# Kernel optimization log

Hardware: AMD Instinct MI355X
Metric: run time of the kernel (lower is better)

## Reference

```python
import jax, jax.numpy as jnp
import numpy as np

D_MODEL = 1024
NUM_HEADS = 16
DEPTH = D_MODEL // NUM_HEADS


def setup_inputs() -> dict:
    key = jax.random.key(0)
    ks = jax.random.split(key, 10)
    B, LQ, LK = 4, 2048, 2048
    # xavier_uniform bound for square [d,d] weight
    bound = float(np.sqrt(6.0 / (D_MODEL + D_MODEL)))
    def w(k):
        return jax.random.uniform(k, (D_MODEL, D_MODEL), jnp.float32, -bound, bound)
    return {
        "query": jax.random.normal(ks[0], (B, LQ, D_MODEL), jnp.float32),
        "value": jax.random.normal(ks[1], (B, LK, D_MODEL), jnp.float32),
        "wq": w(ks[2]), "bq": jnp.zeros((D_MODEL,), jnp.float32),
        "wk": w(ks[3]), "bk": jnp.zeros((D_MODEL,), jnp.float32),
        "wv": w(ks[4]), "bv": jnp.zeros((D_MODEL,), jnp.float32),
        "wo": w(ks[5]), "bo": jnp.zeros((D_MODEL,), jnp.float32),
    }


def _split_heads(x, B):
    # [B, L, d_model] -> [B, H, L, depth]
    return x.reshape(B, -1, NUM_HEADS, DEPTH).transpose(0, 2, 1, 3)


def reference(query, value, wq, bq, wk, bk, wv, bv, wo, bo):
    B = query.shape[0]
    # torch nn.Linear: y = x @ W.T + b
    q = _split_heads(query @ wq.T + bq, B)          # [B,H,Lq,depth]
    k = _split_heads(value @ wk.T + bk, B)          # [B,H,Lk,depth]
    v = _split_heads(value @ wv.T + bv, B)          # [B,H,Lk,depth]
    scale = jnp.sqrt(jnp.asarray(DEPTH, dtype=q.dtype))
    scores = jnp.einsum("bhqd,bhkd->bhqk", q, k) / scale
    attn = jax.nn.softmax(scores, axis=-1)
    ctx = jnp.einsum("bhqk,bhkd->bhqd", attn, v)    # [B,H,Lq,depth]
    ctx = ctx.transpose(0, 2, 1, 3).reshape(B, -1, D_MODEL)
    return ctx @ wo.T + bo
```

## Files before the change

kernel.cpp:

```cpp
#include <hip/hip_runtime.h>
#include <hip/hip_bf16.h>

typedef unsigned short u16;
typedef unsigned int u32;
typedef __attribute__((ext_vector_type(8))) short bf16x8;
typedef __attribute__((ext_vector_type(4))) float f32x4;

#define MFMA16(a, b, c) __builtin_amdgcn_mfma_f32_16x16x32_bf16(a, b, c, 0, 0, 0)

#define QSCALE 0.18033688011112042f

__device__ inline u16 f2b(float f) {
    union { float f; unsigned int i; } v;
    v.f = f;
    unsigned int r = v.i + 0x7fffu + ((v.i >> 16) & 1u);
    return (u16)(r >> 16);
}
__device__ inline u32 fbits(float f) {
    union { float f; u32 i; } v; v.f = f; return v.i;
}
__device__ inline u32 pack2_trunc(float f0, float f1) {
    return __builtin_amdgcn_perm(fbits(f1), fbits(f0), 0x07060302u);
}

__device__ inline void glds16(const u16* g, u16* l) {
    __builtin_amdgcn_global_load_lds(
        (const __attribute__((address_space(1))) unsigned int*)g,
        (__attribute__((address_space(3))) unsigned int*)l, 16, 0, 0);
}

__global__ __launch_bounds__(256) void cvt_all(
    const float* __restrict__ q, const float* __restrict__ v,
    const float* __restrict__ wq, const float* __restrict__ wk,
    const float* __restrict__ wv, const float* __restrict__ wo,
    u16* __restrict__ qb, u16* __restrict__ vb,
    u16* __restrict__ wqb, u16* __restrict__ wkb,
    u16* __restrict__ wvb, u16* __restrict__ wob)
{
    int flat = blockIdx.x;
    const float* x; u16* y; int off;
    if (flat < 8192) {
        x = flat < 4096 ? q : v;
        y = flat < 4096 ? qb : vb;
        off = flat & 4095;
    } else {
        int s = (flat - 8192) >> 9;
        off = (flat - 8192) & 511;
        x = s == 0 ? wq : (s == 1 ? wk : (s == 2 ? wv : wo));
        y = s == 0 ? wqb : (s == 1 ? wkb : (s == 2 ? wvb : wob));
    }
    int i = (off * 256 + threadIdx.x) * 8;
    float4 a = *(const float4*)(x + i);
    float4 b = *(const float4*)(x + i + 4);
    u16 o[8] = { f2b(a.x), f2b(a.y), f2b(a.z), f2b(a.w),
                 f2b(b.x), f2b(b.y), f2b(b.z), f2b(b.w) };
    *(uint4*)(y + i) = *(uint4*)o;
}

__global__ __launch_bounds__(256) void gemm_proj(
    const u16* __restrict__ qb, const u16* __restrict__ vb,
    const u16* __restrict__ wqb, const u16* __restrict__ wkb,
    const u16* __restrict__ wvb,
    const float* __restrict__ bq, const float* __restrict__ bk,
    const float* __restrict__ bv,
    u16* __restrict__ Qp, u16* __restrict__ Kp, u16* __restrict__ Vp,
    int M, int K)
{
    const int flat = blockIdx.x;
    const int xcd = flat & 7, idx = flat >> 3;
    const int mt  = xcd * 8 + (idx & 7);
    const int yy  = idx >> 3;
    const int sel = yy >> 3;
    const int n0 = (yy & 7) * 128;
    const u16* A = sel ? vb : qb;
    const u16* W = sel == 0 ? wqb : (sel == 1 ? wkb : wvb);
    const float* bias = sel == 0 ? bq : (sel == 1 ? bk : bv);
    u16* C = sel == 0 ? Qp : (sel == 1 ? Kp : Vp);
    const float cscale = sel == 0 ? QSCALE : 1.0f;

    __shared__ __align__(16) u16 As[128 * 32];
    __shared__ __align__(16) u16 Bs[128 * 32];

    const int tid  = threadIdx.x;
    const int wave = tid >> 6, lane = tid & 63;
    const int quad = lane >> 4, l16 = lane & 15;
    const int m0 = mt * 128;
    const int wm = (wave >> 1) * 64, wn = (wave & 1) * 64;
    const int r0 = lane >> 2;
    const int c0 = (lane & 3) * 8;

    f32x4 acc[4][4] = {};

    for (int k0 = 0; k0 < K; k0 += 32) {
        __syncthreads();
        {
            int ra = wave * 16 + r0;
            glds16(&A[(size_t)(m0 + ra) * K + k0 + c0],      &As[ra * 32 + c0]);
            glds16(&A[(size_t)(m0 + 64 + ra) * K + k0 + c0], &As[(64 + ra) * 32 + c0]);
            glds16(&W[(size_t)(n0 + ra) * K + k0 + c0],      &Bs[ra * 32 + c0]);
            glds16(&W[(size_t)(n0 + 64 + ra) * K + k0 + c0], &Bs[(64 + ra) * 32 + c0]);
        }
        __syncthreads();

        bf16x8 af[4], bfr[4];
#pragma unroll
        for (int mi = 0; mi < 4; ++mi)
            af[mi] = *(const bf16x8*)(&As[(wm + mi * 16 + l16) * 32 + quad * 8]);
#pragma unroll
        for (int ni = 0; ni < 4; ++ni)
            bfr[ni] = *(const bf16x8*)(&Bs[(wn + ni * 16 + l16) * 32 + quad * 8]);
#pragma unroll
        for (int mi = 0; mi < 4; ++mi)
#pragma unroll
            for (int ni = 0; ni < 4; ++ni)
                acc[mi][ni] = MFMA16(af[mi], bfr[ni], acc[mi][ni]);
    }

#pragma unroll
    for (int mi = 0; mi < 4; ++mi) {
#pragma unroll
        for (int ni = 0; ni < 4; ++ni) {
            int col = n0 + wn + ni * 16 + l16;
            float bv2 = bias[col];
#pragma unroll
            for (int r = 0; r < 4; ++r) {
                int row = m0 + wm + mi * 16 + quad * 4 + r;
                C[(size_t)row * 1024 + col] = f2b((acc[mi][ni][r] + bv2) * cscale);
            }
        }
    }
}

__global__ __launch_bounds__(256) void gemm_out(
    const u16* __restrict__ A, const u16* __restrict__ B,
    const float* __restrict__ bias, float* __restrict__ C,
    int M, int N, int K)
{
    __shared__ __align__(16) u16 As[128 * 32];
    __shared__ __align__(16) u16 Bs[128 * 32];

    const int flat = blockIdx.x;
    const int xcd = flat & 7, idx = flat >> 3;
    const int mt  = xcd * 8 + (idx & 7);
    const int m0 = mt * 128, n0 = (idx >> 3) * 128;

    const int tid  = threadIdx.x;
    const int wave = tid >> 6, lane = tid & 63;
    const int quad = lane >> 4, l16 = lane & 15;
    const int wm = (wave >> 1) * 64, wn = (wave & 1) * 64;
    const int r0 = lane >> 2;
    const int c0 = (lane & 3) * 8;

    f32x4 acc[4][4] = {};

    for (int k0 = 0; k0 < K; k0 += 32) {
        __syncthreads();
        {
            int ra = wave * 16 + r0;
            glds16(&A[(size_t)(m0 + ra) * K + k0 + c0],      &As[ra * 32 + c0]);
            glds16(&A[(size_t)(m0 + 64 + ra) * K + k0 + c0], &As[(64 + ra) * 32 + c0]);
            glds16(&B[(size_t)(n0 + ra) * K + k0 + c0],      &Bs[ra * 32 + c0]);
            glds16(&B[(size_t)(n0 + 64 + ra) * K + k0 + c0], &Bs[(64 + ra) * 32 + c0]);
        }
        __syncthreads();

        bf16x8 af[4], bfr[4];
#pragma unroll
        for (int mi = 0; mi < 4; ++mi)
            af[mi] = *(const bf16x8*)(&As[(wm + mi * 16 + l16) * 32 + quad * 8]);
#pragma unroll
        for (int ni = 0; ni < 4; ++ni)
            bfr[ni] = *(const bf16x8*)(&Bs[(wn + ni * 16 + l16) * 32 + quad * 8]);
#pragma unroll
        for (int mi = 0; mi < 4; ++mi)
#pragma unroll
            for (int ni = 0; ni < 4; ++ni)
                acc[mi][ni] = MFMA16(af[mi], bfr[ni], acc[mi][ni]);
    }

#pragma unroll
    for (int mi = 0; mi < 4; ++mi) {
#pragma unroll
        for (int ni = 0; ni < 4; ++ni) {
            int col = n0 + wn + ni * 16 + l16;
            float bv = bias[col];
#pragma unroll
            for (int r = 0; r < 4; ++r) {
                int row = m0 + wm + mi * 16 + quad * 4 + r;
                C[(size_t)row * N + col] = acc[mi][ni][r] + bv;
            }
        }
    }
}

__global__ __launch_bounds__(256) void transpose_v(
    const u16* __restrict__ Vp, u16* __restrict__ VT)
{
    __shared__ u16 T[64 * 66];
    const int tid = threadIdx.x;
    const int l0 = blockIdx.x * 64, d0 = blockIdx.y * 64, b = blockIdx.z;

#pragma unroll
    for (int i = 0; i < 2; ++i) {
        int ch = tid + i * 256;
        int lrow = ch >> 3, c8 = (ch & 7) * 8;
        uint4 vv = *(const uint4*)(&Vp[((size_t)b * 2048 + l0 + lrow) * 1024 + d0 + c8]);
        const u16* vp = (const u16*)&vv;
#pragma unroll
        for (int j = 0; j < 8; ++j) T[lrow * 66 + c8 + j] = vp[j];
    }
    __syncthreads();
#pragma unroll
    for (int i = 0; i < 2; ++i) {
        int ch = tid + i * 256;
        int drow = ch >> 3, l8 = (ch & 7) * 8;
        u16 o[8];
#pragma unroll
        for (int j = 0; j < 8; ++j) o[j] = T[(l8 + j) * 66 + drow];
        *(uint4*)(&VT[((size_t)b * 1024 + d0 + drow) * 2048 + l0 + l8]) = *(uint4*)o;
    }
}

__global__ __launch_bounds__(256, 4) void attn(
    const u16* __restrict__ Q, const u16* __restrict__ K,
    const u16* __restrict__ VT, u16* __restrict__ O,
    int LQ, int LK)
{
    const int tid  = threadIdx.x;
    const int wave = tid >> 6, lane = tid & 63;
    const int quad = lane >> 4, l16 = lane & 15;
    const int flat = blockIdx.x;
    const int xcd = flat & 7, slot = flat >> 3;
    const int bh = xcd * 8 + (slot >> 4);
    const int q0 = (slot & 15) * 128;
    const int b = bh >> 4, h = bh & 15;
    const size_t qbase = ((size_t)b * LQ + q0) * 1024 + h * 64;
    const size_t kbase = ((size_t)b * LK) * 1024 + h * 64;
    const size_t vtbase = ((size_t)b * 1024 + h * 64) * 2048;

    __shared__ __align__(16) u16 Ks[64 * 72];
    __shared__ __align__(16) u16 VTs[64 * 72];
    __shared__ __align__(16) u16 Ps[4][32 * 40];

    bf16x8 qf[2][2];
#pragma unroll
    for (int mi = 0; mi < 2; ++mi)
#pragma unroll
        for (int ks = 0; ks < 2; ++ks)
            qf[mi][ks] = *(const bf16x8*)(
                &Q[qbase + (size_t)(wave * 32 + mi * 16 + l16) * 1024 + ks * 32 + quad * 8]);

    const bf16x8 vones = { 0x3F80, 0x3F80, 0x3F80, 0x3F80,
                           0x3F80, 0x3F80, 0x3F80, 0x3F80 };

    f32x4 oacc[2][5] = {};

    for (int kt = 0; kt < LK; kt += 64) {
        __syncthreads();
#pragma unroll
        for (int i = 0; i < 2; ++i) {
            int ch = tid + i * 256;
            int row = ch >> 3, c8 = (ch & 7) * 8;
            *(uint4*)(&Ks[row * 72 + c8]) =
                *(const uint4*)(&K[kbase + (size_t)(kt + row) * 1024 + c8]);
            *(uint4*)(&VTs[row * 72 + c8]) =
                *(const uint4*)(&VT[vtbase + (size_t)row * 2048 + kt + c8]);
        }
        __syncthreads();

        f32x4 st[4][2] = {};
#pragma unroll
        for (int ks = 0; ks < 2; ++ks) {
            bf16x8 kf[4];
#pragma unroll
            for (int ni = 0; ni < 4; ++ni)
                kf[ni] = *(const bf16x8*)(&Ks[(ni * 16 + l16) * 72 + ks * 32 + quad * 8]);
            __builtin_amdgcn_s_setprio(1);
#pragma unroll
            for (int ni = 0; ni < 4; ++ni)
#pragma unroll
                for (int mi = 0; mi < 2; ++mi)
                    st[ni][mi] = MFMA16(kf[ni], qf[mi][ks], st[ni][mi]);
            __builtin_amdgcn_s_setprio(0);
        }

#pragma unroll
        for (int ks = 0; ks < 2; ++ks) {
#pragma unroll
            for (int mi = 0; mi < 2; ++mi)
#pragma unroll
                for (int ni2 = 0; ni2 < 2; ++ni2) {
                    const f32x4 s4 = st[ks * 2 + ni2][mi];
                    float p0 = __builtin_amdgcn_exp2f(s4[0]);
                    float p1 = __builtin_amdgcn_exp2f(s4[1]);
                    float p2 = __builtin_amdgcn_exp2f(s4[2]);
                    float p3 = __builtin_amdgcn_exp2f(s4[3]);
                    uint2 w;
                    w.x = pack2_trunc(p0, p1);
                    w.y = pack2_trunc(p2, p3);
                    *(uint2*)(&Ps[wave][(mi * 16 + l16) * 40 + ni2 * 16 + quad * 4]) = w;
                }

            bf16x8 vf[4];
#pragma unroll
            for (int nd = 0; nd < 4; ++nd)
                vf[nd] = *(const bf16x8*)(&VTs[(nd * 16 + l16) * 72 + ks * 32 + quad * 8]);
            __builtin_amdgcn_s_setprio(1);
#pragma unroll
            for (int mi = 0; mi < 2; ++mi) {
                bf16x8 pf = *(const bf16x8*)(&Ps[wave][(mi * 16 + l16) * 40 + quad * 8]);
#pragma unroll
                for (int nd = 0; nd < 4; ++nd)
                    oacc[mi][nd] = MFMA16(pf, vf[nd], oacc[mi][nd]);
                oacc[mi][4] = MFMA16(pf, vones, oacc[mi][4]);
            }
            __builtin_amdgcn_s_setprio(0);
        }
    }

#pragma unroll
    for (int mi = 0; mi < 2; ++mi)
#pragma unroll
        for (int r = 0; r < 4; ++r) {
            float inv = 1.0f / oacc[mi][4][r];
            int row = q0 + wave * 32 + mi * 16 + quad * 4 + r;
            size_t rb = ((size_t)b * LQ + row) * 1024 + h * 64;
#pragma unroll
            for (int nd = 0; nd < 4; ++nd)
                O[rb + nd * 16 + l16] = f2b(oacc[mi][nd][r] * inv);
        }
}

extern "C" void kernel_launch(void* const* d_in, const int* in_sizes, int n_in,
                              void* d_out, int out_size, void* d_ws, size_t ws_size,
                              hipStream_t stream) {
    const float* query = (const float*)d_in[0];
    const float* value = (const float*)d_in[1];
    const float* wq = (const float*)d_in[2];
    const float* bq = (const float*)d_in[3];
    const float* wk = (const float*)d_in[4];
    const float* bk = (const float*)d_in[5];
    const float* wv = (const float*)d_in[6];
    const float* bv = (const float*)d_in[7];
    const float* wo = (const float*)d_in[8];
    const float* bo = (const float*)d_in[9];

    const int B = 4, LQ = 2048, LK = 2048, D = 1024;
    const int M = B * LQ;
    const int mat = M * D;
    const int wsz = D * D;

    u16* ws  = (u16*)d_ws;
    u16* qb  = ws;
    u16* vb  = qb + mat;
    u16* wqb = vb + mat;
    u16* wkb = wqb + wsz;
    u16* wvb = wkb + wsz;
    u16* wob = wvb + wsz;
    u16* Qp  = wob + wsz;
    u16* Kp  = Qp + mat;
    u16* Vp  = Kp + mat;
    u16* VT  = Vp + mat;
    u16* Cp  = Vp;

    dim3 blk(256);

    cvt_all<<<dim3(10240), blk, 0, stream>>>(
        query, value, wq, wk, wv, wo, qb, vb, wqb, wkb, wvb, wob);

    gemm_proj<<<dim3(1536), blk, 0, stream>>>(
        qb, vb, wqb, wkb, wvb, bq, bk, bv, Qp, Kp, Vp, M, D);

    transpose_v<<<dim3(32, 16, 4), blk, 0, stream>>>(Vp, VT);

    attn<<<dim3(1024), blk, 0, stream>>>(Qp, Kp, VT, Cp, LQ, LK);

    gemm_out<<<dim3(512), blk, 0, stream>>>(Cp, wob, bo, (float*)d_out, M, D, D);
}
```

Baseline: 328.5 us.

## Fuse V transpose into projection epilogue and compute softmax row sums in VALU

The V projection GEMM now writes its output already transposed (VT layout) with 4-element packed stores, so the separate transpose_v kernel and its extra read/write pass over V disappear. Separately, the attention kernel drops the extra MFMA against a ones vector that produced the softmax denominator. It instead accumulates per-lane row sums of the truncated bf16 probabilities in registers and reduces them with cross-lane shuffles at the end. The risks are strided 8-byte stores in the GEMM epilogue and extra VALU work in the attention inner loop.

```diff
diff --git a/kernel.cpp b/kernel.cpp
--- a/kernel.cpp
+++ b/kernel.cpp
@@ -18,6 +18,9 @@
 }
 __device__ inline u32 fbits(float f) {
     union { float f; u32 i; } v; v.f = f; return v.i;
+}
+__device__ inline float bfloat(u32 b) {
+    union { u32 i; float f; } v; v.i = b; return v.f;
 }
 __device__ inline u32 pack2_trunc(float f0, float f1) {
     return __builtin_amdgcn_perm(fbits(f1), fbits(f0), 0x07060302u);
@@ -63,7 +66,7 @@
     const u16* __restrict__ wvb,
     const float* __restrict__ bq, const float* __restrict__ bk,
     const float* __restrict__ bv,
-    u16* __restrict__ Qp, u16* __restrict__ Kp, u16* __restrict__ Vp,
+    u16* __restrict__ Qp, u16* __restrict__ Kp, u16* __restrict__ VT,
     int M, int K)
 {
     const int flat = blockIdx.x;
@@ -75,7 +78,6 @@
     const u16* A = sel ? vb : qb;
     const u16* W = sel == 0 ? wqb : (sel == 1 ? wkb : wvb);
     const float* bias = sel == 0 ? bq : (sel == 1 ? bk : bv);
-    u16* C = sel == 0 ? Qp : (sel == 1 ? Kp : Vp);
     const float cscale = sel == 0 ? QSCALE : 1.0f;
 
     __shared__ __align__(16) u16 As[128 * 32];
@@ -116,16 +118,34 @@
                 acc[mi][ni] = MFMA16(af[mi], bfr[ni], acc[mi][ni]);
     }
 
-#pragma unroll
-    for (int mi = 0; mi < 4; ++mi) {
-#pragma unroll
-        for (int ni = 0; ni < 4; ++ni) {
-            int col = n0 + wn + ni * 16 + l16;
-            float bv2 = bias[col];
-#pragma unroll
-            for (int r = 0; r < 4; ++r) {
-                int row = m0 + wm + mi * 16 + quad * 4 + r;
-                C[(size_t)row * 1024 + col] = f2b((acc[mi][ni][r] + bv2) * cscale);
+    if (sel == 2) {
+#pragma unroll
+        for (int mi = 0; mi < 4; ++mi) {
+#pragma unroll
+            for (int ni = 0; ni < 4; ++ni) {
+                int col = n0 + wn + ni * 16 + l16;
+                float bv2 = bias[col];
+                int row0 = m0 + wm + mi * 16 + quad * 4;
+                int bb = row0 >> 11, l0 = row0 & 2047;
+                u16 o[4];
+#pragma unroll
+                for (int r = 0; r < 4; ++r) o[r] = f2b(acc[mi][ni][r] + bv2);
+                *(uint2*)(&VT[((size_t)bb * 1024 + col) * 2048 + l0]) = *(uint2*)o;
+            }
+        }
+    } else {
+        u16* C = sel == 0 ? Qp : Kp;
+#pragma unroll
+        for (int mi = 0; mi < 4; ++mi) {
+#pragma unroll
+            for (int ni = 0; ni < 4; ++ni) {
+                int col = n0 + wn + ni * 16 + l16;
+                float bv2 = bias[col];
+#pragma unroll
+                for (int r = 0; r < 4; ++r) {
+                    int row = m0 + wm + mi * 16 + quad * 4 + r;
+                    C[(size_t)row * 1024 + col] = f2b((acc[mi][ni][r] + bv2) * cscale);
+                }
             }
         }
     }
@@ -190,34 +210,6 @@
                 C[(size_t)row * N + col] = acc[mi][ni][r] + bv;
             }
         }
-    }
-}
-
-__global__ __launch_bounds__(256) void transpose_v(
-    const u16* __restrict__ Vp, u16* __restrict__ VT)
-{
-    __shared__ u16 T[64 * 66];
-    const int tid = threadIdx.x;
-    const int l0 = blockIdx.x * 64, d0 = blockIdx.y * 64, b = blockIdx.z;
-
-#pragma unroll
-    for (int i = 0; i < 2; ++i) {
-        int ch = tid + i * 256;
-        int lrow = ch >> 3, c8 = (ch & 7) * 8;
-        uint4 vv = *(const uint4*)(&Vp[((size_t)b * 2048 + l0 + lrow) * 1024 + d0 + c8]);
-        const u16* vp = (const u16*)&vv;
-#pragma unroll
-        for (int j = 0; j < 8; ++j) T[lrow * 66 + c8 + j] = vp[j];
-    }
-    __syncthreads();
-#pragma unroll
-    for (int i = 0; i < 2; ++i) {
-        int ch = tid + i * 256;
-        int drow = ch >> 3, l8 = (ch & 7) * 8;
-        u16 o[8];
-#pragma unroll
-        for (int j = 0; j < 8; ++j) o[j] = T[(l8 + j) * 66 + drow];
-        *(uint4*)(&VT[((size_t)b * 1024 + d0 + drow) * 2048 + l0 + l8]) = *(uint4*)o;
     }
 }
 
@@ -250,10 +242,8 @@
             qf[mi][ks] = *(const bf16x8*)(
                 &Q[qbase + (size_t)(wave * 32 + mi * 16 + l16) * 1024 + ks * 32 + quad * 8]);
 
-    const bf16x8 vones = { 0x3F80, 0x3F80, 0x3F80, 0x3F80,
-                           0x3F80, 0x3F80, 0x3F80, 0x3F80 };
-
-    f32x4 oacc[2][5] = {};
+    f32x4 oacc[2][4] = {};
+    float rsum[2] = {0.0f, 0.0f};
 
     for (int kt = 0; kt < LK; kt += 64) {
         __syncthreads();
@@ -299,6 +289,8 @@
                     w.x = pack2_trunc(p0, p1);
                     w.y = pack2_trunc(p2, p3);
                     *(uint2*)(&Ps[wave][(mi * 16 + l16) * 40 + ni2 * 16 + quad * 4]) = w;
+                    rsum[mi] += (bfloat(w.x << 16) + bfloat(w.x & 0xffff0000u))
+                              + (bfloat(w.y << 16) + bfloat(w.y & 0xffff0000u));
                 }
 
             bf16x8 vf[4];
@@ -312,17 +304,26 @@
 #pragma unroll
                 for (int nd = 0; nd < 4; ++nd)
                     oacc[mi][nd] = MFMA16(pf, vf[nd], oacc[mi][nd]);
-                oacc[mi][4] = MFMA16(pf, vones, oacc[mi][4]);
             }
             __builtin_amdgcn_s_setprio(0);
         }
     }
 
+    float rs[2];
+#pragma unroll
+    for (int mi = 0; mi < 2; ++mi) {
+        float r = rsum[mi];
+        r += __shfl_xor(r, 16);
+        r += __shfl_xor(r, 32);
+        rs[mi] = r;
+    }
+
 #pragma unroll
     for (int mi = 0; mi < 2; ++mi)
 #pragma unroll
         for (int r = 0; r < 4; ++r) {
-            float inv = 1.0f / oacc[mi][4][r];
+            float den = __shfl(rs[mi], quad * 4 + r);
+            float inv = 1.0f / den;
             int row = q0 + wave * 32 + mi * 16 + quad * 4 + r;
             size_t rb = ((size_t)b * LQ + row) * 1024 + h * 64;
 #pragma unroll
@@ -359,9 +360,8 @@
     u16* wob = wvb + wsz;
     u16* Qp  = wob + wsz;
     u16* Kp  = Qp + mat;
-    u16* Vp  = Kp + mat;
-    u16* VT  = Vp + mat;
-    u16* Cp  = Vp;
+    u16* Cp  = Kp + mat;
+    u16* VT  = Cp + mat;
 
     dim3 blk(256);
 
@@ -369,9 +369,7 @@
         query, value, wq, wk, wv, wo, qb, vb, wqb, wkb, wvb, wob);
 
     gemm_proj<<<dim3(1536), blk, 0, stream>>>(
-        qb, vb, wqb, wkb, wvb, bq, bk, bv, Qp, Kp, Vp, M, D);
-
-    transpose_v<<<dim3(32, 16, 4), blk, 0, stream>>>(Vp, VT);
+        qb, vb, wqb, wkb, wvb, bq, bk, bv, Qp, Kp, VT, M, D);
 
     attn<<<dim3(1024), blk, 0, stream>>>(Qp, Kp, VT, Cp, LQ, LK);
 
```

Measured after the change: 322.6 us. No clear change (-1.8%).
